# Kernel optimization log

Hardware: AMD Instinct MI355X
Metric: run time of the kernel (lower is better)

## Reference

```python
import jax, jax.numpy as jnp
import numpy as np

N_HEADS = 8


def setup_inputs() -> dict:
    key = jax.random.key(0)
    ks = jax.random.split(key, 6)
    B, U, Lx, Ly = 16, 512, 1024, 1024
    x = jax.random.normal(ks[0], (B, U, Lx), dtype=jnp.float32)
    y = jax.random.normal(ks[1], (B, U, Ly), dtype=jnp.float32)
    xy_mask = jax.random.randint(ks[2], (B, Lx, Ly), 0, 2).astype(jnp.bool_)
    wq = jax.random.normal(ks[3], (U, U), dtype=jnp.float32) * (1.0 / np.sqrt(U))
    wk = jax.random.normal(ks[4], (U, U), dtype=jnp.float32) * (1.0 / np.sqrt(U))
    wo = jax.random.normal(ks[5], (U, U), dtype=jnp.float32) * (1.0 / np.sqrt(U))
    return {"x": x, "y": y, "xy_mask": xy_mask, "wq": wq, "wk": wk, "wo": wo}


def reference(x, y, xy_mask, wq, wk, wo):
    # x: (B, U, Lx), y: (B, U, Ly), xy_mask: (B, Lx, Ly)
    B, U, Lx = x.shape
    Ly = y.shape[2]
    H = N_HEADS
    d = U // H
    scale = 1.0 / (d ** 0.5)

    # 1x1 conv (bias=False) == channel-mixing matmul; weight layout (out, in)
    Q = jnp.einsum('ou,bul->bol', wq, x)   # (B, U, Lx)
    K = jnp.einsum('ou,bul->bol', wk, y)   # (B, U, Ly)

    # split channels into heads (head-major channel order, matching torch.split)
    Qh = Q.reshape(B, H, d, Lx)
    Kh = K.reshape(B, H, d, Ly)

    # ReLU-scored attention with mask (no softmax)
    A = jnp.einsum('bhdx,bhdy->bhxy', Qh, Kh)           # (B, H, Lx, Ly)
    A = jnp.maximum(A, 0.0) * scale
    A = jnp.where(xy_mask[:, None, :, :], A, 0.0)

    C = jnp.einsum('bhxy,bhdy->bhdx', A, Kh).reshape(B, U, Lx)

    # per-row element-count normalization (rows with zero count use 1)
    n_el = jnp.maximum(jnp.sum(xy_mask, axis=2), 1)     # (B, Lx)
    C = C / n_el[:, None, :].astype(x.dtype)

    E = 0.5 * (Q + C)
    return jnp.einsum('ou,bul->bol', wo, E)
```

## Files before the change

### kernel.cpp

```cpp
#include <hip/hip_runtime.h>
#include <stdint.h>
#include <stddef.h>

#define B_  16
#define U_  512
#define LX_ 1024
#define LY_ 1024
#define H_  8
#define D_  64

typedef unsigned short ushort_t;
typedef unsigned int   uint_t;
typedef __bf16 v8bf  __attribute__((ext_vector_type(8)));
typedef float  v16f  __attribute__((ext_vector_type(16)));

__device__ __forceinline__ ushort_t bf16u(float f) {
    uint_t u = __float_as_uint(f);
    uint_t r = (u + 0x7FFFu + ((u >> 16) & 1u)) >> 16;
    return (ushort_t)r;
}
__device__ __forceinline__ float bfu2f(ushort_t u) {
    return __uint_as_float(((uint_t)u) << 16);
}
__device__ __forceinline__ void gload16(const void* g, void* l) {
    auto gp = (const __attribute__((address_space(1))) uint32_t*)(uintptr_t)g;
    auto lp = (__attribute__((address_space(3))) uint32_t*)(uintptr_t)l;
    __builtin_amdgcn_global_load_lds(gp, lp, 16, 0, 0);
}

__global__ __launch_bounds__(256) void prep_kernel(const float* __restrict__ X,
                                                   const float* __restrict__ Y,
                                                   const void* __restrict__ mask,
                                                   const float* __restrict__ wq,
                                                   const float* __restrict__ wk,
                                                   const float* __restrict__ wo,
                                                   ushort_t* __restrict__ XT,
                                                   ushort_t* __restrict__ YT,
                                                   ushort_t* __restrict__ wqb,
                                                   ushort_t* __restrict__ wkb,
                                                   ushort_t* __restrict__ wob,
                                                   float* __restrict__ nel,
                                                   uint_t* __restrict__ mb) {
    __shared__ ushort_t T[64][72];
    __shared__ int s;
    const int tid = threadIdx.x;
    const int bid = blockIdx.x;

    if (bid < 4096) {
        const int l0 = (bid & 15) * 64;
        const int u0 = ((bid >> 4) & 7) * 64;
        const int z  = bid >> 7;
        const int b  = z & 15;
        const int sel = z >> 4;
        const float* S = sel ? Y : X;
        ushort_t*  Dst = sel ? YT : XT;
        #pragma unroll
        for (int e = 0; e < 4; ++e) {
            int ci = e * 256 + tid;
            int r = ci >> 4, c4 = (ci & 15) * 4;
            float4 v = *(const float4*)&S[((size_t)(b * U_ + u0 + r) << 10) + l0 + c4];
            T[r][c4 + 0] = bf16u(v.x); T[r][c4 + 1] = bf16u(v.y);
            T[r][c4 + 2] = bf16u(v.z); T[r][c4 + 3] = bf16u(v.w);
        }
        __syncthreads();
        #pragma unroll
        for (int e = 0; e < 2; ++e) {
            int ci = e * 256 + tid;
            int lr = ci >> 3, cc = ci & 7;
            ushort_t tmp[8];
            #pragma unroll
            for (int j = 0; j < 8; ++j) tmp[j] = T[cc * 8 + j][lr];
            *(uint4*)&Dst[((size_t)((b << 10) + l0 + lr)) * U_ + u0 + cc * 8] = *(uint4*)tmp;
        }
    } else if (bid < 8192) {
        const uint_t* mw = (const uint_t*)mask;
        if (tid == 0) s = 0;
        __syncthreads();
        int c = 0;
        for (int i = tid; i < 1024; i += 256) c += (mw[i] <= 1u) ? 1 : 0;
        atomicAdd(&s, c);
        __syncthreads();
        const int isInt = (s >= 1000) ? 1 : 0;

        int row  = (bid - 4096) * 4 + (tid >> 6);
        int lane = tid & 63;
        const uint8_t* m8  = (const uint8_t*)mask + (size_t)row * LY_;
        const int*     m32 = (const int*)mask + (size_t)row * LY_;
        int cnt = 0;
        for (int yg = 0; yg < LY_ / 64; ++yg) {
            int yy = yg * 64 + lane;
            bool p = isInt ? (m32[yy] != 0) : (m8[yy] != 0);
            unsigned long long bal = __ballot(p);
            if (lane == 0) {
                mb[(size_t)row * 32 + yg * 2]     = (uint_t)bal;
                mb[(size_t)row * 32 + yg * 2 + 1] = (uint_t)(bal >> 32);
                cnt += __popcll(bal);
            }
        }
        if (lane == 0) nel[row] = (float)(cnt > 0 ? cnt : 1);
    } else {
        int cb = bid - 8192;
        int selw = cb >> 8;
        const float* sw = selw == 0 ? wq : (selw == 1 ? wk : wo);
        ushort_t*    dw = selw == 0 ? wqb : (selw == 1 ? wkb : wob);
        int i = ((cb & 255) * 256 + tid) * 4;
        float4 v = *(const float4*)&sw[i];
        ushort4 p;
        p.x = bf16u(v.x); p.y = bf16u(v.y); p.z = bf16u(v.z); p.w = bf16u(v.w);
        *(ushort4*)&dw[i] = p;
    }
}

__global__ __launch_bounds__(256) void gemm_qk(const ushort_t* __restrict__ xT,
                                               const ushort_t* __restrict__ wqb,
                                               const ushort_t* __restrict__ wkb,
                                               const ushort_t* __restrict__ yT,
                                               ushort_t* __restrict__ QT,
                                               ushort_t* __restrict__ Ka,
                                               ushort_t* __restrict__ Kb) {
    __shared__ __align__(16) ushort_t As[128 * 64];
    __shared__ __align__(16) ushort_t Bs[128 * 64];
    const int tid = threadIdx.x;
    const int id  = blockIdx.x;
    const int isK = id >> 9;
    const int lid = id & 511;
    const int b   = lid >> 5;
    int m0, n0, ldOut;
    const ushort_t *Ab, *Bb;
    ushort_t* Ob;
    if (!isK) {
        n0 = (lid & 3) * 128; m0 = ((lid >> 2) & 7) * 128;
        Ab = xT + (size_t)b * (LX_ * U_); Bb = wqb;
        Ob = QT + (size_t)b * (LX_ * U_); ldOut = U_;
    } else {
        n0 = (lid & 7) * 128; m0 = ((lid >> 3) & 3) * 128;
        Ab = wkb; Bb = yT + (size_t)b * (LY_ * U_);
        Ob = Ka + (size_t)b * (U_ * LY_); ldOut = LY_;
    }

    const int w = tid >> 6, lane = tid & 63, lo = lane & 31, hi = lane >> 5;
    const int wm = (w >> 1) * 64, wn = (w & 1) * 64;

    v16f acc00, acc01, acc10, acc11;
    #pragma unroll
    for (int i = 0; i < 16; ++i) { acc00[i] = 0.f; acc01[i] = 0.f; acc10[i] = 0.f; acc11[i] = 0.f; }

    for (int kk = 0; kk < 8; ++kk) {
        const int k0 = kk * 64;
        #pragma unroll
        for (int e = 0; e < 4; ++e) {
            int ci = e * 256 + tid;
            int r = ci >> 3, c = ci & 7;
            int g = (c ^ (r & 7)) << 3;
            gload16(&Ab[(size_t)(m0 + r) * U_ + k0 + g], &As[ci * 8]);
            gload16(&Bb[(size_t)(n0 + r) * U_ + k0 + g], &Bs[ci * 8]);
        }
        __syncthreads();
        #pragma unroll
        for (int ks = 0; ks < 4; ++ks) {
            int ch = ks * 2 + hi;
            int rA0 = wm + lo, rA1 = wm + 32 + lo;
            int rB0 = wn + lo, rB1 = wn + 32 + lo;
            v8bf a0 = *(v8bf*)&As[rA0 * 64 + ((ch ^ (rA0 & 7)) << 3)];
            v8bf a1 = *(v8bf*)&As[rA1 * 64 + ((ch ^ (rA1 & 7)) << 3)];
            v8bf b0 = *(v8bf*)&Bs[rB0 * 64 + ((ch ^ (rB0 & 7)) << 3)];
            v8bf b1 = *(v8bf*)&Bs[rB1 * 64 + ((ch ^ (rB1 & 7)) << 3)];
            acc00 = __builtin_amdgcn_mfma_f32_32x32x16_bf16(a0, b0, acc00, 0, 0, 0);
            acc01 = __builtin_amdgcn_mfma_f32_32x32x16_bf16(a0, b1, acc01, 0, 0, 0);
            acc10 = __builtin_amdgcn_mfma_f32_32x32x16_bf16(a1, b0, acc10, 0, 0, 0);
            acc11 = __builtin_amdgcn_mfma_f32_32x32x16_bf16(a1, b1, acc11, 0, 0, 0);
        }
        __syncthreads();
    }

    #pragma unroll
    for (int mi = 0; mi < 2; ++mi) {
        #pragma unroll
        for (int nj = 0; nj < 2; ++nj) {
            v16f c = mi ? (nj ? acc11 : acc10) : (nj ? acc01 : acc00);
            int n = n0 + wn + nj * 32 + lo;
            #pragma unroll
            for (int r = 0; r < 16; ++r) {
                int m = m0 + wm + mi * 32 + (r & 3) + 8 * (r >> 2) + 4 * hi;
                ushort_t v = bf16u(c[r]);
                Ob[(size_t)m * ldOut + n] = v;
                if (isK)
                    Kb[(((size_t)(b * H_ + (m >> 6)) << 10) + n) * D_ + (m & 63)] = v;
            }
        }
    }
}

template <int OUTF32>
__global__ __launch_bounds__(256) void gemm_mfma(const ushort_t* __restrict__ A, size_t aStr,
                                                 const ushort_t* __restrict__ Bm, size_t bStr,
                                                 void* __restrict__ Out, size_t oStr, int ldOut) {
    const int n0 = blockIdx.x * 128;
    const int m0 = blockIdx.y * 128;
    const int b  = blockIdx.z;
    __shared__ __align__(16) ushort_t As[128 * 64];
    __shared__ __align__(16) ushort_t Bs[128 * 64];
    const int tid = threadIdx.x;
    const ushort_t* Ab = A + aStr * b;
    const ushort_t* Bb = Bm + bStr * b;

    const int w = tid >> 6, lane = tid & 63, lo = lane & 31, hi = lane >> 5;
    const int wm = (w >> 1) * 64, wn = (w & 1) * 64;

    v16f acc00, acc01, acc10, acc11;
    #pragma unroll
    for (int i = 0; i < 16; ++i) { acc00[i] = 0.f; acc01[i] = 0.f; acc10[i] = 0.f; acc11[i] = 0.f; }

    for (int kk = 0; kk < 8; ++kk) {
        const int k0 = kk * 64;
        #pragma unroll
        for (int e = 0; e < 4; ++e) {
            int ci = e * 256 + tid;
            int r = ci >> 3, c = ci & 7;
            int g = (c ^ (r & 7)) << 3;
            gload16(&Ab[(size_t)(m0 + r) * U_ + k0 + g], &As[ci * 8]);
            gload16(&Bb[(size_t)(n0 + r) * U_ + k0 + g], &Bs[ci * 8]);
        }
        __syncthreads();
        #pragma unroll
        for (int ks = 0; ks < 4; ++ks) {
            int ch = ks * 2 + hi;
            int rA0 = wm + lo, rA1 = wm + 32 + lo;
            int rB0 = wn + lo, rB1 = wn + 32 + lo;
            v8bf a0 = *(v8bf*)&As[rA0 * 64 + ((ch ^ (rA0 & 7)) << 3)];
            v8bf a1 = *(v8bf*)&As[rA1 * 64 + ((ch ^ (rA1 & 7)) << 3)];
            v8bf b0 = *(v8bf*)&Bs[rB0 * 64 + ((ch ^ (rB0 & 7)) << 3)];
            v8bf b1 = *(v8bf*)&Bs[rB1 * 64 + ((ch ^ (rB1 & 7)) << 3)];
            acc00 = __builtin_amdgcn_mfma_f32_32x32x16_bf16(a0, b0, acc00, 0, 0, 0);
            acc01 = __builtin_amdgcn_mfma_f32_32x32x16_bf16(a0, b1, acc01, 0, 0, 0);
            acc10 = __builtin_amdgcn_mfma_f32_32x32x16_bf16(a1, b0, acc10, 0, 0, 0);
            acc11 = __builtin_amdgcn_mfma_f32_32x32x16_bf16(a1, b1, acc11, 0, 0, 0);
        }
        __syncthreads();
    }

    #pragma unroll
    for (int mi = 0; mi < 2; ++mi) {
        #pragma unroll
        for (int nj = 0; nj < 2; ++nj) {
            v16f c = mi ? (nj ? acc11 : acc10) : (nj ? acc01 : acc00);
            int n = n0 + wn + nj * 32 + lo;
            #pragma unroll
            for (int r = 0; r < 16; ++r) {
                int m = m0 + wm + mi * 32 + (r & 3) + 8 * (r >> 2) + 4 * hi;
                size_t addr = oStr * b + (size_t)m * ldOut + n;
                if (OUTF32) ((float*)Out)[addr] = c[r];
                else        ((ushort_t*)Out)[addr] = bf16u(c[r]);
            }
        }
    }
}

typedef uint_t v2u __attribute__((ext_vector_type(2)));

__device__ __forceinline__ void conv_sblock(const v16f& s, uint_t wbh, v8bf* fr) {
    uint_t pk[8];
    #pragma unroll
    for (int i = 0; i < 8; ++i) {
        float f0 = fmaxf(s[2 * i + 0], 0.f);
        float f1 = fmaxf(s[2 * i + 1], 0.f);
        uint_t r;
        asm("v_cvt_pk_bf16_f32 %0, %1, %2" : "=v"(r) : "v"(f0), "v"(f1));
        pk[i] = r;
    }
    #pragma unroll
    for (int t = 0; t < 2; ++t) {
        auto ra = __builtin_amdgcn_permlane32_swap(pk[4 * t + 0], pk[4 * t + 2], false, false);
        auto rb = __builtin_amdgcn_permlane32_swap(pk[4 * t + 1], pk[4 * t + 3], false, false);
        uint_t w0 = ra[0];
        uint_t w1 = rb[0];
        uint_t w2 = ra[1];
        uint_t w3 = rb[1];
        uint_t u0 = wbh >> (t * 16 + 0);
        uint_t u1 = wbh >> (t * 16 + 2);
        uint_t u2 = wbh >> (t * 16 + 4);
        uint_t u3 = wbh >> (t * 16 + 6);
        w0 &= ((u0 & 1u) * 0xFFFFu) | ((u0 & 2u) * 0x7FFF8000u);
        w1 &= ((u1 & 1u) * 0xFFFFu) | ((u1 & 2u) * 0x7FFF8000u);
        w2 &= ((u2 & 1u) * 0xFFFFu) | ((u2 & 2u) * 0x7FFF8000u);
        w3 &= ((u3 & 1u) * 0xFFFFu) | ((u3 & 2u) * 0x7FFF8000u);
        union { uint_t u[4]; v8bf b; } cv;
        cv.u[0] = w0; cv.u[1] = w1; cv.u[2] = w2; cv.u[3] = w3;
        fr[t] = cv.b;
    }
}

__global__ __launch_bounds__(256, 4) void attn_mfma(const ushort_t* __restrict__ QTg,
                                                    const ushort_t* __restrict__ Ka_g,
                                                    const ushort_t* __restrict__ Kb_g,
                                                    const uint_t* __restrict__ mbits,
                                                    const float* __restrict__ nel,
                                                    ushort_t* __restrict__ ETg) {
    const int tid = threadIdx.x;
    const int id  = blockIdx.x;
    const int bh  = id & 127;
    const int x0g = (id >> 7) * 128;
    const int b = bh >> 3, h = bh & 7;

    __shared__ __align__(16) ushort_t SM[4 * 4096];

    const int w    = tid >> 6;
    const int lane = tid & 63;
    const int lo   = lane & 31;
    const int hi   = lane >> 5;
    const int xq   = w * 32;

    const ushort_t* KaBase = Ka_g + ((size_t)(b * U_ + h * D_)) * LY_;
    const ushort_t* KbBase = Kb_g + ((size_t)(b * H_ + h)) * LY_ * D_;
    const int bx = b * LX_ + x0g;
    const int xg = bx + xq + lo;

    #pragma unroll
    for (int e = 0; e < 2; ++e) {
        int ci = e * 256 + tid;
        int r = ci >> 3, c = ci & 7;
        int g8 = (c ^ (r & 7)) << 3;
        gload16(&KbBase[(size_t)r * D_ + g8], &SM[ci * 8]);
        gload16(&KaBase[(size_t)r * LY_ + g8], &SM[8192 + ci * 8]);
    }

    v8bf qf[4];
    {
        const ushort_t* q0 = QTg + (size_t)xg * U_ + h * D_;
        #pragma unroll
        for (int kt = 0; kt < 4; ++kt) qf[kt] = *(const v8bf*)&q0[(kt * 2 + hi) * 8];
    }

    v16f acc0, acc1;
    #pragma unroll
    for (int i = 0; i < 16; ++i) { acc0[i] = 0.f; acc1[i] = 0.f; }

    __syncthreads();

    for (int tt = 0; tt < 16; ++tt) {
        ushort_t* KBc = SM + (tt & 1) * 4096;
        ushort_t* KAc = SM + 8192 + (tt & 1) * 4096;

        if (tt < 15) {
            ushort_t* KBn = SM + ((tt + 1) & 1) * 4096;
            ushort_t* KAn = SM + 8192 + ((tt + 1) & 1) * 4096;
            const int yn = tt * 64 + 64;
            #pragma unroll
            for (int e = 0; e < 2; ++e) {
                int ci = e * 256 + tid;
                int r = ci >> 3, c = ci & 7;
                int g8 = (c ^ (r & 7)) << 3;
                gload16(&KbBase[(size_t)(yn + r) * D_ + g8], &KBn[ci * 8]);
                gload16(&KaBase[(size_t)r * LY_ + yn + g8], &KAn[ci * 8]);
            }
        }
        v2u wb = *(const v2u*)&mbits[(size_t)xg * 32 + tt * 2];

        v8bf fr0[2], fr1[2];
        {
            v16f s;
            #pragma unroll
            for (int i = 0; i < 16; ++i) s[i] = 0.f;
            #pragma unroll
            for (int kt = 0; kt < 4; ++kt) {
                int ch = kt * 2 + hi;
                v8bf a = *(v8bf*)&KBc[lo * 64 + ((ch ^ (lo & 7)) << 3)];
                s = __builtin_amdgcn_mfma_f32_32x32x16_bf16(a, qf[kt], s, 0, 0, 0);
            }
            conv_sblock(s, wb[0] >> (hi * 8), fr0);
        }
        {
            v16f s;
            #pragma unroll
            for (int i = 0; i < 16; ++i) s[i] = 0.f;
            #pragma unroll
            for (int kt = 0; kt < 4; ++kt) {
                int ch = kt * 2 + hi;
                v8bf a = *(v8bf*)&KBc[(32 + lo) * 64 + ((ch ^ ((32 + lo) & 7)) << 3)];
                s = __builtin_amdgcn_mfma_f32_32x32x16_bf16(a, qf[kt], s, 0, 0, 0);
            }
            conv_sblock(s, wb[1] >> (hi * 8), fr1);
        }

        #pragma unroll
        for (int kt = 0; kt < 4; ++kt) {
            int ch = kt * 2 + hi;
            v8bf frk = (kt < 2) ? fr0[kt] : fr1[kt - 2];
            v8bf a0 = *(v8bf*)&KAc[lo * 64 + ((ch ^ (lo & 7)) << 3)];
            v8bf a1 = *(v8bf*)&KAc[(32 + lo) * 64 + ((ch ^ ((32 + lo) & 7)) << 3)];
            acc0 = __builtin_amdgcn_mfma_f32_32x32x16_bf16(a0, frk, acc0, 0, 0, 0);
            acc1 = __builtin_amdgcn_mfma_f32_32x32x16_bf16(a1, frk, acc1, 0, 0, 0);
        }
        __syncthreads();
    }

    {
        ushort_t* Et = SM;
        const int xl = xq + lo;
        float invn = 0.0625f / nel[xg];
        const ushort_t* qg = QTg + (size_t)xg * U_ + h * D_ + 4 * hi;
        #pragma unroll
        for (int half = 0; half < 2; ++half) {
            const v16f& c = half ? acc1 : acc0;
            #pragma unroll
            for (int q = 0; q < 4; ++q) {
                int d0 = half * 32 + q * 8 + 4 * hi;
                ushort_t q4[4];
                *(uint2*)q4 = *(const uint2*)&qg[half * 32 + q * 8];
                ushort_t e4[4];
                e4[0] = bf16u(0.5f * bfu2f(q4[0]) + c[q * 4 + 0] * invn);
                e4[1] = bf16u(0.5f * bfu2f(q4[1]) + c[q * 4 + 1] * invn);
                e4[2] = bf16u(0.5f * bfu2f(q4[2]) + c[q * 4 + 2] * invn);
                e4[3] = bf16u(0.5f * bfu2f(q4[3]) + c[q * 4 + 3] * invn);
                int base = xl * 64 + ((((d0 >> 3) ^ (xl & 7)) << 3) | (4 * hi));
                *(uint2*)&Et[base] = *(uint2*)e4;
            }
        }
    }
    __syncthreads();
    #pragma unroll
    for (int e = 0; e < 4; ++e) {
        int idx = e * 256 + tid;
        int row = idx >> 3, cc = idx & 7;
        uint4 v = *(const uint4*)&SM[row * 64 + ((cc ^ (row & 7)) << 3)];
        *(uint4*)&ETg[((size_t)(bx + row)) * U_ + h * D_ + cc * 8] = v;
    }
}

extern "C" void kernel_launch(void* const* d_in, const int* in_sizes, int n_in,
                              void* d_out, int out_size, void* d_ws, size_t ws_size,
                              hipStream_t stream) {
    const float* x    = (const float*)d_in[0];
    const float* y    = (const float*)d_in[1];
    const void*  mask = d_in[2];
    const float* wq   = (const float*)d_in[3];
    const float* wk   = (const float*)d_in[4];
    const float* wo   = (const float*)d_in[5];

    char* wsb = (char*)d_ws;
    ushort_t* xT    = (ushort_t*)(wsb);
    ushort_t* yT    = (ushort_t*)(wsb + 16777216);
    ushort_t* Ka    = (ushort_t*)(wsb + 33554432);
    ushort_t* wqb   = (ushort_t*)(wsb + 50331648);
    ushort_t* wkb   = (ushort_t*)(wsb + 50855936);
    ushort_t* wob   = (ushort_t*)(wsb + 51380224);
    uint_t*   mbits = (uint_t*)(wsb + 51904512);
    float*    nel   = (float*)(wsb + 54001664);
    ushort_t* ET    = xT;
    ushort_t* QT    = (ushort_t*)d_out;
    ushort_t* Kb    = (ushort_t*)d_out + (size_t)B_ * LX_ * U_;

    prep_kernel<<<8960, 256, 0, stream>>>(x, y, mask, wq, wk, wo,
                                          xT, yT, wqb, wkb, wob, nel, mbits);
    gemm_qk<<<1024, 256, 0, stream>>>(xT, wqb, wkb, yT, QT, Ka, Kb);
    attn_mfma<<<1024, 256, 0, stream>>>(QT, Ka, Kb, mbits, nel, ET);
    gemm_mfma<1><<<dim3(8, 4, B_), 256, 0, stream>>>(
        wob, 0, ET, (size_t)LX_ * U_, d_out, (size_t)U_ * LX_, LX_);
}
```

Measured before the change: 288.4 us.

## Pack bf16 pairs in prep transpose, vectorize K stores, simplify mask-type detection

```diff
diff --git a/kernel.cpp b/kernel.cpp
--- a/kernel.cpp
+++ b/kernel.cpp
@@ -21,6 +21,12 @@
 }
 __device__ __forceinline__ float bfu2f(ushort_t u) {
     return __uint_as_float(((uint_t)u) << 16);
+}
+__device__ __forceinline__ uint_t pkbf16(float f0, float f1) {
+    uint_t u0 = __float_as_uint(f0), u1 = __float_as_uint(f1);
+    u0 = u0 + 0x7FFFu + ((u0 >> 16) & 1u);
+    u1 = u1 + 0x7FFFu + ((u1 >> 16) & 1u);
+    return __builtin_amdgcn_perm(u1, u0, 0x07060302u);
 }
 __device__ __forceinline__ void gload16(const void* g, void* l) {
     auto gp = (const __attribute__((address_space(1))) uint32_t*)(uintptr_t)g;
@@ -41,8 +47,7 @@
                                                    ushort_t* __restrict__ wob,
                                                    float* __restrict__ nel,
                                                    uint_t* __restrict__ mb) {
-    __shared__ ushort_t T[64][72];
-    __shared__ int s;
+    __shared__ uint_t Tp[64 * 33];
     const int tid = threadIdx.x;
     const int bid = blockIdx.x;
 
@@ -59,42 +64,55 @@
             int ci = e * 256 + tid;
             int r = ci >> 4, c4 = (ci & 15) * 4;
             float4 v = *(const float4*)&S[((size_t)(b * U_ + u0 + r) << 10) + l0 + c4];
-            T[r][c4 + 0] = bf16u(v.x); T[r][c4 + 1] = bf16u(v.y);
-            T[r][c4 + 2] = bf16u(v.z); T[r][c4 + 3] = bf16u(v.w);
+            Tp[r * 33 + (c4 >> 1)]     = pkbf16(v.x, v.y);
+            Tp[r * 33 + (c4 >> 1) + 1] = pkbf16(v.z, v.w);
         }
         __syncthreads();
         #pragma unroll
         for (int e = 0; e < 2; ++e) {
             int ci = e * 256 + tid;
             int lr = ci >> 3, cc = ci & 7;
-            ushort_t tmp[8];
-            #pragma unroll
-            for (int j = 0; j < 8; ++j) tmp[j] = T[cc * 8 + j][lr];
-            *(uint4*)&Dst[((size_t)((b << 10) + l0 + lr)) * U_ + u0 + cc * 8] = *(uint4*)tmp;
+            int l2 = lr >> 1;
+            uint_t sel8 = (lr & 1) ? 0x07060302u : 0x05040100u;
+            uint_t wv[4];
+            #pragma unroll
+            for (int i = 0; i < 4; ++i) {
+                uint_t A  = Tp[(cc * 8 + 2 * i) * 33 + l2];
+                uint_t Bv = Tp[(cc * 8 + 2 * i + 1) * 33 + l2];
+                wv[i] = __builtin_amdgcn_perm(Bv, A, sel8);
+            }
+            *(uint4*)&Dst[((size_t)((b << 10) + l0 + lr)) * U_ + u0 + cc * 8] = *(uint4*)wv;
         }
     } else if (bid < 8192) {
-        const uint_t* mw = (const uint_t*)mask;
-        if (tid == 0) s = 0;
-        __syncthreads();
-        int c = 0;
-        for (int i = tid; i < 1024; i += 256) c += (mw[i] <= 1u) ? 1 : 0;
-        atomicAdd(&s, c);
-        __syncthreads();
-        const int isInt = (s >= 1000) ? 1 : 0;
+        const int lane = tid & 63;
+        const uint4* m4 = (const uint4*)mask;
+        uint4 dw = m4[lane];
+        bool all4 = (dw.x <= 1u) && (dw.y <= 1u) && (dw.z <= 1u) && (dw.w <= 1u);
+        const int isInt = (__popcll(__ballot(all4)) >= 32) ? 1 : 0;
 
         int row  = (bid - 4096) * 4 + (tid >> 6);
-        int lane = tid & 63;
         const uint8_t* m8  = (const uint8_t*)mask + (size_t)row * LY_;
         const int*     m32 = (const int*)mask + (size_t)row * LY_;
         int cnt = 0;
-        for (int yg = 0; yg < LY_ / 64; ++yg) {
-            int yy = yg * 64 + lane;
-            bool p = isInt ? (m32[yy] != 0) : (m8[yy] != 0);
-            unsigned long long bal = __ballot(p);
-            if (lane == 0) {
-                mb[(size_t)row * 32 + yg * 2]     = (uint_t)bal;
-                mb[(size_t)row * 32 + yg * 2 + 1] = (uint_t)(bal >> 32);
-                cnt += __popcll(bal);
+        if (isInt) {
+            #pragma unroll 4
+            for (int yg = 0; yg < LY_ / 64; ++yg) {
+                unsigned long long bal = __ballot(m32[yg * 64 + lane] != 0);
+                if (lane == 0) {
+                    mb[(size_t)row * 32 + yg * 2]     = (uint_t)bal;
+                    mb[(size_t)row * 32 + yg * 2 + 1] = (uint_t)(bal >> 32);
+                    cnt += __popcll(bal);
+                }
+            }
+        } else {
+            #pragma unroll 4
+            for (int yg = 0; yg < LY_ / 64; ++yg) {
+                unsigned long long bal = __ballot(m8[yg * 64 + lane] != 0);
+                if (lane == 0) {
+                    mb[(size_t)row * 32 + yg * 2]     = (uint_t)bal;
+                    mb[(size_t)row * 32 + yg * 2 + 1] = (uint_t)(bal >> 32);
+                    cnt += __popcll(bal);
+                }
             }
         }
         if (lane == 0) nel[row] = (float)(cnt > 0 ? cnt : 1);
@@ -179,13 +197,26 @@
         for (int nj = 0; nj < 2; ++nj) {
             v16f c = mi ? (nj ? acc11 : acc10) : (nj ? acc01 : acc00);
             int n = n0 + wn + nj * 32 + lo;
+            int mbase = m0 + wm + mi * 32;
+            ushort_t us[16];
             #pragma unroll
             for (int r = 0; r < 16; ++r) {
-                int m = m0 + wm + mi * 32 + (r & 3) + 8 * (r >> 2) + 4 * hi;
+                int m = mbase + (r & 3) + 8 * (r >> 2) + 4 * hi;
                 ushort_t v = bf16u(c[r]);
+                us[r] = v;
                 Ob[(size_t)m * ldOut + n] = v;
-                if (isK)
-                    Kb[(((size_t)(b * H_ + (m >> 6)) << 10) + n) * D_ + (m & 63)] = v;
+            }
+            if (isK) {
+                int head = mbase >> 6;
+                int db   = (mbase & 63) + 4 * hi;
+                ushort_t* kbrow = Kb + (((size_t)(b * H_ + head) << 10) + n) * D_ + db;
+                #pragma unroll
+                for (int q = 0; q < 4; ++q) {
+                    uint2 pk2;
+                    pk2.x = (uint_t)us[q * 4 + 0] | ((uint_t)us[q * 4 + 1] << 16);
+                    pk2.y = (uint_t)us[q * 4 + 2] | ((uint_t)us[q * 4 + 3] << 16);
+                    *(uint2*)&kbrow[q * 8] = pk2;
+                }
             }
         }
     }
@@ -337,6 +368,7 @@
 
     __syncthreads();
 
+    #pragma unroll 2
     for (int tt = 0; tt < 16; ++tt) {
         ushort_t* KBc = SM + (tt & 1) * 4096;
         ushort_t* KAc = SM + 8192 + (tt & 1) * 4096;
```

After: 279.3 us. -3.2%, faster.
